# Kernel optimization log

Hardware: AMD Instinct MI355X
Metric: run time of the kernel (lower is better)

Reference implementation:

```python
import jax, jax.numpy as jnp
import numpy as np

B, T, M, P = 256, 256, 256, 256  # batch, timesteps, encoder hidden m, decoder hidden p


def setup_inputs() -> dict:
    key = jax.random.key(0)
    ks = jax.random.split(key, 12)
    def n(k, shape, s=0.05):
        return jax.random.normal(k, shape, dtype=jnp.float32) * s
    return {
        "data": n(ks[0], (B, T - 1, 1), 1.0),          # decoder inputs y_1..y_{T-1}
        "encoder_h": n(ks[1], (B, T, M), 1.0),          # encoder hidden states
        "h0": jnp.zeros((B, P), jnp.float32),
        "s0": jnp.zeros((B, P), jnp.float32),
        # dense: Dense(1) on concat([x, context]) -> input dim 1+M
        "Wd": n(ks[2], (1 + M, 1)), "bd": jnp.zeros((1,), jnp.float32),
        # decoder LSTM (Keras gate order i,f,c,o): kernel (1,4P), recurrent (P,4P)
        "Wk": n(ks[3], (1, 4 * P)), "Wr": n(ks[4], (P, 4 * P)), "bl": jnp.zeros((4 * P,), jnp.float32),
        # temporal attention: W: 2P->M, U: M->M, v: M->1
        "Ww": n(ks[5], (2 * P, M)), "bw": jnp.zeros((M,), jnp.float32),
        "Wu": n(ks[6], (M, M)), "bu": jnp.zeros((M,), jnp.float32),
        "Wv": n(ks[7], (M, 1)), "bv": jnp.zeros((1,), jnp.float32),
        # output head: densevb: P+M -> 1, denseWb: 1 -> P
        "Wvb": n(ks[8], (P + M, 1)), "bvb": jnp.zeros((1,), jnp.float32),
        "Wwb": n(ks[9], (1, P)), "bwb": jnp.zeros((P,), jnp.float32),
    }


def reference(data, encoder_h, h0, s0, Wd, bd, Wk, Wr, bl, Ww, bw,
              Wu, bu, Wv, bv, Wvb, bvb, Wwb, bwb):
    # Hoist U(encoder_h) out of the time loop: it does not depend on t (same math).
    Ue = encoder_h @ Wu + bu                      # (B, T, M)
    xs = jnp.transpose(data, (1, 0, 2))           # (T-1, B, 1) for scan
    ctx0 = jnp.zeros((data.shape[0], Ue.shape[-1]), data.dtype)  # initial context (B, M)

    def step(carry, x_t):
        h, s, ctx = carry                          # (B,P), (B,P), (B,M)
        # y_tilde = Dense(1)(concat([x_t, context]))
        y = jnp.concatenate([x_t, ctx], axis=-1) @ Wd + bd        # (B, 1)
        # single-step Keras LSTM cell, gates i, f, c, o
        z = y @ Wk + h @ Wr + bl                   # (B, 4P)
        i, f, g, o = jnp.split(z, 4, axis=-1)
        s_new = jax.nn.sigmoid(f) * s + jax.nn.sigmoid(i) * jnp.tanh(g)
        h_new = jax.nn.sigmoid(o) * jnp.tanh(s_new)
        # temporal attention: l = v(tanh(W(repeat(concat[h,s])) + U(encoder_h)))
        dsc = jnp.concatenate([h_new, s_new], axis=-1) @ Ww + bw  # (B, M)
        l = jnp.tanh(dsc[:, None, :] + Ue) @ Wv + bv              # (B, T, 1)
        beta = jax.nn.softmax(l, axis=1)                          # softmax over time axis
        # context = beta^T @ encoder_h -> (B, M)
        ctx_new = jnp.sum(beta * encoder_h, axis=1)
        return (h_new, s_new, ctx_new), None

    (h, s, ctx), _ = jax.lax.scan(step, (h0, s0, ctx0), xs)
    cat = jnp.concatenate([h, ctx], axis=-1)[:, None, :]          # (B, 1, P+M)
    # denseWb(densevb(concatenated)): (P+M)->1 then 1->P, as in the source
    return (cat @ Wvb + bvb) @ Wwb + bwb                          # (B, 1, P)
```

## Files before the change

### kernel.cpp

```cpp
#include <hip/hip_runtime.h>
#include <hip/hip_bf16.h>

#define B 256
#define T 256
#define M 256
#define P 256
#define TSTEPS 255
#define NT 1024
#define RG 6

typedef unsigned int uint;
typedef _Float16 hf2 __attribute__((ext_vector_type(2)));

#define KEEP4(v) asm volatile("" : "+v"((v).x), "+v"((v).y), "+v"((v).z), "+v"((v).w))

__device__ __forceinline__ float fast_tanh(float x) {
    float e = exp2f(x * 2.885390082f);
    return 1.f - 2.f * __builtin_amdgcn_rcpf(e + 1.f);
}
__device__ __forceinline__ float fast_sigmoid(float x) {
    float e = exp2f(-x * 1.442695041f);
    return __builtin_amdgcn_rcpf(1.f + e);
}

#if defined(__has_builtin)
#if __has_builtin(__builtin_amdgcn_fdot2)
#define HAVE_FDOT2 1
#endif
#endif

__device__ __forceinline__ float dot2(uint a, uint b, float c) {
#ifdef HAVE_FDOT2
    return __builtin_amdgcn_fdot2(__builtin_bit_cast(hf2, a),
                                  __builtin_bit_cast(hf2, b), c, false);
#else
    hf2 x = __builtin_bit_cast(hf2, a), y = __builtin_bit_cast(hf2, b);
    return c + (float)x.x * (float)y.x + (float)x.y * (float)y.y;
#endif
}

__device__ __forceinline__ uint pk16(float a, float b) {
    return __builtin_bit_cast(uint, __builtin_amdgcn_cvt_pkrtz(a, b));
}

__device__ __forceinline__ uint pkmulsq(uint a, uint b) {
    uint p;
    asm("v_pk_mul_f16 %0, %1, %2\n\t"
        "v_pk_mul_f16 %0, %0, %0" : "=v"(p) : "v"(a), "v"(b));
    return p;
}

__device__ __forceinline__ float rcp1p(float x) {
    return __builtin_amdgcn_rcpf(x + 1.f);
}

__global__ __launch_bounds__(256) void ue_gemm(
    const float* __restrict__ enc, const float* __restrict__ Wu,
    const float* __restrict__ bu, _Float16* __restrict__ Ue16)
{
    __shared__ float At[32][256];
    const int r0 = blockIdx.x * 32;
    const int tid = threadIdx.x;

    #pragma unroll 4
    for (int i = 0; i < 32; ++i)
        At[i][tid] = enc[(size_t)(r0 + i) * 256 + tid];
    __syncthreads();

    float acc[32];
    #pragma unroll
    for (int r = 0; r < 32; ++r) acc[r] = 0.f;

    for (int k = 0; k < 256; k += 4) {
        float w0 = Wu[(size_t)(k + 0) * 256 + tid];
        float w1 = Wu[(size_t)(k + 1) * 256 + tid];
        float w2 = Wu[(size_t)(k + 2) * 256 + tid];
        float w3 = Wu[(size_t)(k + 3) * 256 + tid];
        #pragma unroll
        for (int r = 0; r < 32; ++r) {
            float4 a4 = *(const float4*)&At[r][k];
            acc[r] += a4.x * w0 + a4.y * w1 + a4.z * w2 + a4.w * w3;
        }
    }
    float bub = bu[tid];
    #pragma unroll 4
    for (int r = 0; r < 32; ++r)
        Ue16[(size_t)(r0 + r) * 256 + tid] =
            (_Float16)exp2f(1.442695041f * (acc[r] + bub));
}

__global__ __launch_bounds__(256) void wr_cvt(
    const float* __restrict__ Wr, uint4* __restrict__ Wsz)
{
    int i = blockIdx.x * 256 + threadIdx.x;
    int kc = i >> 10, c = i & 1023;
    const float* s = Wr + (size_t)kc * 8 * 1024 + c;
    uint4 o;
    o.x = pk16(s[0 * 1024], s[1 * 1024]);
    o.y = pk16(s[2 * 1024], s[3 * 1024]);
    o.z = pk16(s[4 * 1024], s[5 * 1024]);
    o.w = pk16(s[6 * 1024], s[7 * 1024]);
    Wsz[i] = o;
}

__global__ __launch_bounds__(256) void ww_cvt(
    const float* __restrict__ Ww, uint4* __restrict__ Wwsz)
{
    int i = blockIdx.x * 256 + threadIdx.x;
    int kk = i >> 8, m = i & 255;
    const float* s = Ww + (size_t)kk * 8 * 256 + m;
    uint4 o;
    o.x = pk16(s[0 * 256], s[1 * 256]);
    o.y = pk16(s[2 * 256], s[3 * 256]);
    o.z = pk16(s[4 * 256], s[5 * 256]);
    o.w = pk16(s[6 * 256], s[7 * 256]);
    Wwsz[i] = o;
}

__global__ __launch_bounds__(NT, 4) void decoder_scan(
    const float* __restrict__ data,
    const float* __restrict__ h0,  const float* __restrict__ s0,
    const float* __restrict__ Wd,  const float* __restrict__ bd,
    const float* __restrict__ Wk,  const float* __restrict__ bl,
    const float* __restrict__ bw,
    const float* __restrict__ Wv,  const float* __restrict__ bv,
    const float* __restrict__ Wvb, const float* __restrict__ bvb,
    const float* __restrict__ Wwb, const float* __restrict__ bwb,
    const float* __restrict__ enc,
    const _Float16* __restrict__ Ue16g,
    const uint4* __restrict__ Wsz, const uint4* __restrict__ Wwsz,
    float* __restrict__ out)
{
    const int b    = blockIdx.x;
    const int tid  = threadIdx.x;
    const int lane = tid & 63;
    const int wave = tid >> 6;

    __shared__ __align__(16) uint4 ww_lds[2 * 16 * 256];
    __shared__ float h_lds[P], s_lds[P];
    __shared__ __align__(16) uint hs2[128 + 4 + 128];
    __shared__ float z_lds[4 * 257];
    __shared__ __align__(16) uint  edup[2][132];
    __shared__ __align__(16) float wv2dup[2][264];
    __shared__ float el_lds[T];
    __shared__ float g_lds[T];
    __shared__ float ctx_lds[M];
    __shared__ __align__(16) float sred[8], yred[8];
    __shared__ float ya[4];
    __shared__ float data_lds[TSTEPS + 1];
    __shared__ int aflag;

    uint* h2_lds = hs2;
    uint* s2_lds = hs2 + 132;

    {
        #pragma unroll
        for (int k = 0; k < 8; ++k) {
            int l = tid + k * NT;
            int i = l >> 9, r = l & 511, dmm = r >> 1, dk = r & 1;
            ww_lds[l] = Wwsz[((dk * 32 + i) << 8) + dmm];
        }
    }
    if (tid == 0) aflag = 0;
    if (tid < 256) {
        float hv = h0[b * 256 + tid], sv = s0[b * 256 + tid];
        h_lds[tid] = hv; s_lds[tid] = sv; ctx_lds[tid] = 0.f;
        float w2 = 2.f * Wv[tid];
        wv2dup[0][tid] = w2; wv2dup[1][tid] = w2;
        float hv1 = __shfl_down(hv, 1, 64);
        float sv1 = __shfl_down(sv, 1, 64);
        if (!(tid & 1)) {
            h2_lds[tid >> 1] = pk16(hv, hv1);
            s2_lds[tid >> 1] = pk16(sv, sv1);
        }
    }
    if (tid < 8) { sred[tid] = 1.f; yred[tid] = 0.f; }
    if (tid < TSTEPS) data_lds[tid] = data[b * TSTEPS + tid];

    const float Wd0 = Wd[0], bd0 = bd[0];
    const float* encB = enc + (size_t)b * T * M;

    {
        float w0 = Wd[1 + lane * 4], w1 = Wd[2 + lane * 4];
        float w2 = Wd[3 + lane * 4], w3 = Wd[4 + lane * 4];
        for (int i = 0; i < 16; ++i) {
            int tp = wave * 16 + i;
            float4 e4 = *(const float4*)&encB[(size_t)tp * 256 + lane * 4];
            float p = e4.x * w0 + e4.y * w1 + e4.z * w2 + e4.w * w3;
            #pragma unroll
            for (int mm = 32; mm >= 1; mm >>= 1) p += __shfl_xor(p, mm, 64);
            if (lane == 0) g_lds[tp] = p;
        }
    }
    __syncthreads();

    const uint4* h2u4 = (const uint4*)h2_lds;
    const uint4* s2u4 = (const uint4*)s2_lds;

    {
        const uint4* wc = Wsz + tid;
        float acc = 0.f;
        #pragma unroll 4
        for (int kc = 0; kc < 32; ++kc) {
            uint4 w = wc[kc << 10];
            uint4 h = h2u4[kc];
            acc = dot2(w.x, h.x, acc); acc = dot2(w.y, h.y, acc);
            acc = dot2(w.z, h.z, acc); acc = dot2(w.w, h.w, acc);
        }
        z_lds[(tid >> 8) * 257 + (tid & 255)] = acc;
    }
    __syncthreads();

    if (wave < 8) {
        const int gate = tid & 3, uu0 = tid >> 2, uu1 = uu0 + 128;
        const int cz0 = gate * 257 + uu0, cz1 = gate * 257 + uu1;
        const float wk0 = Wk[gate * 256 + uu0], bl0 = bl[gate * 256 + uu0];
        const float wk1 = Wk[gate * 256 + uu1], bl1 = bl[gate * 256 + uu1];
        const int zr = tid >> 8, zc = tid & 255;
        const uint4* wcA = Wsz + tid;
        const uint4* wcB = Wsz + tid + 512;
        uint4 rA[RG], rB[RG];
        #pragma unroll
        for (int kc = 0; kc < RG; ++kc) {
            rA[kc] = wcA[kc << 10]; rB[kc] = wcB[kc << 10];
            KEEP4(rA[kc]); KEEP4(rB[kc]);
        }

        for (int t = 0; t < TSTEPS; ++t) {
            {
                float4 sa = *(const float4*)&sred[0], sb = *(const float4*)&sred[4];
                float4 yaa = *(const float4*)&yred[0], yab = *(const float4*)&yred[4];
                float S = sa.x + sa.y + sa.z + sa.w + sb.x + sb.y + sb.z + sb.w;
                float Y = yaa.x + yaa.y + yaa.z + yaa.w + yab.x + yab.y + yab.z + yab.w;
                float ys = Y * __builtin_amdgcn_rcpf(S) + data_lds[t] * Wd0 + bd0;
                float zc0 = z_lds[cz0] + ys * wk0 + bl0;
                float zc1 = z_lds[cz1] + ys * wk1 + bl1;
                float nl0 = (gate == 2) ? fast_tanh(zc0) : fast_sigmoid(zc0);
                float nl1 = (gate == 2) ? fast_tanh(zc1) : fast_sigmoid(zc1);
                float a1 = __shfl_xor(nl0, 1, 64);
                float a2 = __shfl_xor(nl0, 2, 64);
                float a3 = __shfl_xor(nl0, 3, 64);
                float b1 = __shfl_xor(nl1, 1, 64);
                float b2 = __shfl_xor(nl1, 2, 64);
                float b3 = __shfl_xor(nl1, 3, 64);
                float hn0 = 0.f, sv0 = 0.f, hn1 = 0.f, sv1 = 0.f;
                if (gate == 0) {
                    sv0 = a1 * s_lds[uu0] + nl0 * a2;
                    hn0 = a3 * fast_tanh(sv0);
                    sv1 = b1 * s_lds[uu1] + nl1 * b2;
                    hn1 = b3 * fast_tanh(sv1);
                    s_lds[uu0] = sv0; h_lds[uu0] = hn0;
                    s_lds[uu1] = sv1; h_lds[uu1] = hn1;
                }
                float hd0 = __shfl_down(hn0, 4, 64), sd0 = __shfl_down(sv0, 4, 64);
                float hd1 = __shfl_down(hn1, 4, 64), sd1 = __shfl_down(sv1, 4, 64);
                if ((tid & 7) == 0) {
                    h2_lds[uu0 >> 1] = pk16(hn0, hd0); s2_lds[uu0 >> 1] = pk16(sv0, sd0);
                    h2_lds[uu1 >> 1] = pk16(hn1, hd1); s2_lds[uu1 >> 1] = pk16(sv1, sd1);
                }
            }
            __syncthreads();

            float a0 = 0.f, a1 = 0.f;
            #pragma unroll
            for (int kc = 0; kc < RG; ++kc) {
                uint4 h = h2u4[kc];
                a0 = dot2(rA[kc].x, h.x, a0); a0 = dot2(rA[kc].y, h.y, a0);
                a0 = dot2(rA[kc].z, h.z, a0); a0 = dot2(rA[kc].w, h.w, a0);
                a1 = dot2(rB[kc].x, h.x, a1); a1 = dot2(rB[kc].y, h.y, a1);
                a1 = dot2(rB[kc].z, h.z, a1); a1 = dot2(rB[kc].w, h.w, a1);
            }
            #pragma unroll 4
            for (int kc = RG; kc < 32; ++kc) {
                uint4 wA = wcA[kc << 10], wB = wcB[kc << 10];
                uint4 h = h2u4[kc];
                a0 = dot2(wA.x, h.x, a0); a0 = dot2(wA.y, h.y, a0);
                a0 = dot2(wA.z, h.z, a0); a0 = dot2(wA.w, h.w, a0);
                a1 = dot2(wB.x, h.x, a1); a1 = dot2(wB.y, h.y, a1);
                a1 = dot2(wB.z, h.z, a1); a1 = dot2(wB.w, h.w, a1);
            }
            z_lds[zr * 257 + zc] = a0;
            z_lds[(2 + zr) * 257 + zc] = a1;
            __syncthreads();
        }
    } else {
        const int aw  = wave - 8;
        const int aid = tid - 512;
        const int dm  = aid >> 1;
        const int dkh = aid & 1;
        const float bwm = bw[dm];
        const uint4* wwp  = Wwsz + (dkh << 13) + dm;
        const uint4* wwl  = ww_lds + aid;
        const uint4*  edT = (const uint4*)(&edup[dkh][0]) + (dkh << 4);
        const float4* wvT = (const float4*)(&wv2dup[dkh][0]) + (dkh << 5);
        const uint4* cat4 = dkh ? s2u4 : h2u4;

        uint4 eu[16];
        {
            const uint4* eusrc = (const uint4*)(Ue16g + (size_t)b * T * M) + (aid << 4);
            #pragma unroll
            for (int i = 0; i < 16; ++i) { eu[i] = eusrc[i]; KEEP4(eu[i]); }
        }

        for (int t = 0; t < TSTEPS; ++t) {
            __syncthreads();
            float a = 0.f;
            #pragma unroll 4
            for (int i = 0; i < 16; ++i) {
                uint4 w = wwl[i << 9];
                uint4 c = cat4[i];
                a = dot2(w.x, c.x, a); a = dot2(w.y, c.y, a);
                a = dot2(w.z, c.z, a); a = dot2(w.w, c.w, a);
            }
            #pragma unroll 4
            for (int i = 16; i < 32; ++i) {
                uint4 w = wwp[i << 8];
                uint4 c = cat4[i];
                a = dot2(w.x, c.x, a); a = dot2(w.y, c.y, a);
                a = dot2(w.z, c.z, a); a = dot2(w.w, c.w, a);
            }
            a += __shfl_xor(a, 1, 64);
            float ed = exp2f(1.442695041f * (a + bwm));
            float ed2 = __shfl_xor(ed, 2, 64);
            if ((aid & 3) == 0) {
                uint u = pk16(ed, ed2);
                edup[0][dm >> 1] = u;
                edup[1][dm >> 1] = u;
            }
            __threadfence_block();
            if (lane == 0) atomicAdd(&aflag, 1);
            const int tgt = 8 * (t + 1);
            while (*(volatile int*)&aflag < tgt) __builtin_amdgcn_s_sleep(1);
            __threadfence_block();

            __builtin_amdgcn_s_setprio(1);
            float pl = 0.f;
            #pragma unroll
            for (int jj = 0; jj < 16; ++jj) {
                uint4 u = eu[jj];
                uint4 d = edT[jj];
                float4 wA = wvT[jj * 2], wB = wvT[jj * 2 + 1];
                uint q0 = pkmulsq(u.x, d.x);
                uint q1 = pkmulsq(u.y, d.y);
                uint q2 = pkmulsq(u.z, d.z);
                uint q3 = pkmulsq(u.w, d.w);
                hf2 g0 = __builtin_bit_cast(hf2, q0);
                hf2 g1 = __builtin_bit_cast(hf2, q1);
                hf2 g2 = __builtin_bit_cast(hf2, q2);
                hf2 g3 = __builtin_bit_cast(hf2, q3);
                pl = fmaf(wA.x, rcp1p((float)g0.x), pl);
                pl = fmaf(wA.y, rcp1p((float)g0.y), pl);
                pl = fmaf(wA.z, rcp1p((float)g1.x), pl);
                pl = fmaf(wA.w, rcp1p((float)g1.y), pl);
                pl = fmaf(wB.x, rcp1p((float)g2.x), pl);
                pl = fmaf(wB.y, rcp1p((float)g2.y), pl);
                pl = fmaf(wB.z, rcp1p((float)g3.x), pl);
                pl = fmaf(wB.w, rcp1p((float)g3.y), pl);
            }
            pl += __shfl_xor(pl, 1, 64);
            float ev = exp2f(-1.442695041f * pl);
            if (!dkh) el_lds[dm] = ev;
            float yg = ev * g_lds[dm];
            #pragma unroll
            for (int mm = 2; mm <= 32; mm <<= 1) {
                ev += __shfl_xor(ev, mm, 64);
                yg += __shfl_xor(yg, mm, 64);
            }
            if (lane == 0) { sred[aw] = ev; yred[aw] = yg; }
            __builtin_amdgcn_s_setprio(0);
            __syncthreads();
        }
    }

    {
        float S;
        {
            float4 sa = *(const float4*)&sred[0], sb = *(const float4*)&sred[4];
            S = sa.x + sa.y + sa.z + sa.w + sb.x + sb.y + sb.z + sb.w;
        }
        float a0 = 0.f, a1 = 0.f, a2 = 0.f, a3 = 0.f;
        for (int i = 0; i < 16; ++i) {
            int tp = wave * 16 + i;
            float w = el_lds[tp];
            float4 e4 = *(const float4*)&encB[(size_t)tp * 256 + lane * 4];
            a0 += w * e4.x; a1 += w * e4.y; a2 += w * e4.z; a3 += w * e4.w;
        }
        atomicAdd(&ctx_lds[lane * 4 + 0], a0);
        atomicAdd(&ctx_lds[lane * 4 + 1], a1);
        atomicAdd(&ctx_lds[lane * 4 + 2], a2);
        atomicAdd(&ctx_lds[lane * 4 + 3], a3);
        __syncthreads();

        float qp = 0.f;
        if (tid < 256) {
            float ctx = ctx_lds[tid] * __builtin_amdgcn_rcpf(S);
            qp = h_lds[tid] * Wvb[tid] + ctx * Wvb[256 + tid];
        }
        if (wave < 4) {
            #pragma unroll
            for (int mm = 32; mm >= 1; mm >>= 1) qp += __shfl_xor(qp, mm, 64);
            if (lane == 0) ya[wave] = qp;
        }
        __syncthreads();
        if (tid < 256) {
            float qv = ya[0] + ya[1] + ya[2] + ya[3] + bvb[0];
            out[b * 256 + tid] = qv * Wwb[tid] + bwb[tid];
        }
    }
}

extern "C" void kernel_launch(void* const* d_in, const int* in_sizes, int n_in,
                              void* d_out, int out_size, void* d_ws, size_t ws_size,
                              hipStream_t stream) {
    const float* data = (const float*)d_in[0];
    const float* enc  = (const float*)d_in[1];
    const float* h0   = (const float*)d_in[2];
    const float* s0   = (const float*)d_in[3];
    const float* Wd   = (const float*)d_in[4];
    const float* bd   = (const float*)d_in[5];
    const float* Wk   = (const float*)d_in[6];
    const float* Wr   = (const float*)d_in[7];
    const float* bl   = (const float*)d_in[8];
    const float* Ww   = (const float*)d_in[9];
    const float* bw   = (const float*)d_in[10];
    const float* Wu   = (const float*)d_in[11];
    const float* bu   = (const float*)d_in[12];
    const float* Wv   = (const float*)d_in[13];
    const float* bv   = (const float*)d_in[14];
    const float* Wvb  = (const float*)d_in[15];
    const float* bvb  = (const float*)d_in[16];
    const float* Wwb  = (const float*)d_in[17];
    const float* bwb  = (const float*)d_in[18];

    _Float16* Ue16 = (_Float16*)d_ws;
    uint4* Wsz  = (uint4*)((char*)d_ws + (32ull << 20));
    uint4* Wwsz = (uint4*)((char*)d_ws + (32ull << 20) + (512ull << 10));
    float* out = (float*)d_out;

    hipLaunchKernelGGL(ue_gemm, dim3((B * T) / 32), dim3(256), 0, stream,
                       enc, Wu, bu, Ue16);
    hipLaunchKernelGGL(wr_cvt, dim3(128), dim3(256), 0, stream, Wr, Wsz);
    hipLaunchKernelGGL(ww_cvt, dim3(64), dim3(256), 0, stream, Ww, Wwsz);
    hipLaunchKernelGGL(decoder_scan, dim3(B), dim3(NT), 0, stream,
                       data, h0, s0, Wd, bd, Wk, bl, bw,
                       Wv, bv, Wvb, bvb, Wwb, bwb,
                       enc, Ue16, Wsz, Wwsz, out);
}
```

Baseline: 2.367 ms.

## Replace per-step block barriers with flag-based producer/consumer sync and prefetch weights

Replaces the __syncthreads barriers in the recurrent loop with four LDS counter flags, so the LSTM waves and attention waves signal and wait only on the data each needs. Loads of the next weight chunks are issued before the waits to hide global-memory latency behind the synchronization. The count of recurrent-weight chunks held in registers also rises from 6 to 8. This may cut barrier stalls and let the two wave groups overlap more, at the cost of spin-waiting and higher register pressure.

```diff
diff --git a/kernel.cpp b/kernel.cpp
--- a/kernel.cpp
+++ b/kernel.cpp
@@ -7,7 +7,7 @@
 #define P 256
 #define TSTEPS 255
 #define NT 1024
-#define RG 6
+#define RG 8
 
 typedef unsigned int uint;
 typedef _Float16 hf2 __attribute__((ext_vector_type(2)));
@@ -52,6 +52,15 @@
 
 __device__ __forceinline__ float rcp1p(float x) {
     return __builtin_amdgcn_rcpf(x + 1.f);
+}
+
+__device__ __forceinline__ void fsig(int* f, int lane) {
+    __threadfence_block();
+    if (lane == 0) atomicAdd(f, 1);
+}
+__device__ __forceinline__ void fwait(int* f, int tgt) {
+    while (*(volatile int*)f < tgt) __builtin_amdgcn_s_sleep(1);
+    __threadfence_block();
 }
 
 __global__ __launch_bounds__(256) void ue_gemm(
@@ -148,7 +157,7 @@
     __shared__ __align__(16) float sred[8], yred[8];
     __shared__ float ya[4];
     __shared__ float data_lds[TSTEPS + 1];
-    __shared__ int aflag;
+    __shared__ int pf, zf, ef, df;
 
     uint* h2_lds = hs2;
     uint* s2_lds = hs2 + 132;
@@ -161,7 +170,7 @@
             ww_lds[l] = Wwsz[((dk * 32 + i) << 8) + dmm];
         }
     }
-    if (tid == 0) aflag = 0;
+    if (tid == 0) { pf = 0; zf = 0; ef = 0; df = 0; }
     if (tid < 256) {
         float hv = h0[b * 256 + tid], sv = s0[b * 256 + tid];
         h_lds[tid] = hv; s_lds[tid] = sv; ctx_lds[tid] = 0.f;
@@ -227,6 +236,11 @@
         }
 
         for (int t = 0; t < TSTEPS; ++t) {
+            uint4 pA0 = wcA[(RG + 0) << 10], pB0 = wcB[(RG + 0) << 10];
+            uint4 pA1 = wcA[(RG + 1) << 10], pB1 = wcB[(RG + 1) << 10];
+
+            fwait(&zf, 8 * t);
+            fwait(&ef, 8 * t);
             {
                 float4 sa = *(const float4*)&sred[0], sb = *(const float4*)&sred[4];
                 float4 yaa = *(const float4*)&yred[0], yab = *(const float4*)&yred[4];
@@ -259,7 +273,8 @@
                     h2_lds[uu1 >> 1] = pk16(hn1, hd1); s2_lds[uu1 >> 1] = pk16(sv1, sd1);
                 }
             }
-            __syncthreads();
+            fsig(&pf, lane);
+            fwait(&pf, 8 * (t + 1));
 
             float a0 = 0.f, a1 = 0.f;
             #pragma unroll
@@ -270,8 +285,22 @@
                 a1 = dot2(rB[kc].x, h.x, a1); a1 = dot2(rB[kc].y, h.y, a1);
                 a1 = dot2(rB[kc].z, h.z, a1); a1 = dot2(rB[kc].w, h.w, a1);
             }
+            {
+                uint4 h = h2u4[RG];
+                a0 = dot2(pA0.x, h.x, a0); a0 = dot2(pA0.y, h.y, a0);
+                a0 = dot2(pA0.z, h.z, a0); a0 = dot2(pA0.w, h.w, a0);
+                a1 = dot2(pB0.x, h.x, a1); a1 = dot2(pB0.y, h.y, a1);
+                a1 = dot2(pB0.z, h.z, a1); a1 = dot2(pB0.w, h.w, a1);
+            }
+            {
+                uint4 h = h2u4[RG + 1];
+                a0 = dot2(pA1.x, h.x, a0); a0 = dot2(pA1.y, h.y, a0);
+                a0 = dot2(pA1.z, h.z, a0); a0 = dot2(pA1.w, h.w, a0);
+                a1 = dot2(pB1.x, h.x, a1); a1 = dot2(pB1.y, h.y, a1);
+                a1 = dot2(pB1.z, h.z, a1); a1 = dot2(pB1.w, h.w, a1);
+            }
             #pragma unroll 4
-            for (int kc = RG; kc < 32; ++kc) {
+            for (int kc = RG + 2; kc < 32; ++kc) {
                 uint4 wA = wcA[kc << 10], wB = wcB[kc << 10];
                 uint4 h = h2u4[kc];
                 a0 = dot2(wA.x, h.x, a0); a0 = dot2(wA.y, h.y, a0);
@@ -281,7 +310,7 @@
             }
             z_lds[zr * 257 + zc] = a0;
             z_lds[(2 + zr) * 257 + zc] = a1;
-            __syncthreads();
+            fsig(&zf, lane);
         }
     } else {
         const int aw  = wave - 8;
@@ -303,7 +332,9 @@
         }
 
         for (int t = 0; t < TSTEPS; ++t) {
-            __syncthreads();
+            uint4 e0 = wwp[16 << 8], e1 = wwp[17 << 8];
+            uint4 e2 = wwp[18 << 8], e3 = wwp[19 << 8];
+            fwait(&pf, 8 * (t + 1));
             float a = 0.f;
             #pragma unroll 4
             for (int i = 0; i < 16; ++i) {
@@ -312,8 +343,22 @@
                 a = dot2(w.x, c.x, a); a = dot2(w.y, c.y, a);
                 a = dot2(w.z, c.z, a); a = dot2(w.w, c.w, a);
             }
+            {
+                uint4 c = cat4[16];
+                a = dot2(e0.x, c.x, a); a = dot2(e0.y, c.y, a);
+                a = dot2(e0.z, c.z, a); a = dot2(e0.w, c.w, a);
+                c = cat4[17];
+                a = dot2(e1.x, c.x, a); a = dot2(e1.y, c.y, a);
+                a = dot2(e1.z, c.z, a); a = dot2(e1.w, c.w, a);
+                c = cat4[18];
+                a = dot2(e2.x, c.x, a); a = dot2(e2.y, c.y, a);
+                a = dot2(e2.z, c.z, a); a = dot2(e2.w, c.w, a);
+                c = cat4[19];
+                a = dot2(e3.x, c.x, a); a = dot2(e3.y, c.y, a);
+                a = dot2(e3.z, c.z, a); a = dot2(e3.w, c.w, a);
+            }
             #pragma unroll 4
-            for (int i = 16; i < 32; ++i) {
+            for (int i = 20; i < 32; ++i) {
                 uint4 w = wwp[i << 8];
                 uint4 c = cat4[i];
                 a = dot2(w.x, c.x, a); a = dot2(w.y, c.y, a);
@@ -327,11 +372,8 @@
                 edup[0][dm >> 1] = u;
                 edup[1][dm >> 1] = u;
             }
-            __threadfence_block();
-            if (lane == 0) atomicAdd(&aflag, 1);
-            const int tgt = 8 * (t + 1);
-            while (*(volatile int*)&aflag < tgt) __builtin_amdgcn_s_sleep(1);
-            __threadfence_block();
+            fsig(&df, lane);
+            fwait(&df, 8 * (t + 1));
 
             __builtin_amdgcn_s_setprio(1);
             float pl = 0.f;
@@ -368,9 +410,11 @@
             }
             if (lane == 0) { sred[aw] = ev; yred[aw] = yg; }
             __builtin_amdgcn_s_setprio(0);
-            __syncthreads();
-        }
-    }
+            fsig(&ef, lane);
+        }
+    }
+
+    __syncthreads();
 
     {
         float S;
```

After: 2.395 ms. Within noise of the previous version (+1.2%).
